# Optimization experiments

Measured on AMD Instinct MI355X. Metric: run time of the kernel, lower is better.

The kernel has to match this reference:

```python
import jax, jax.numpy as jnp
import numpy as np

B, C, N, M, H, L = 2, 128, 6000, 1500, 4, 3
DH = C // H


def conv1(x, W, b):
    # 1x1 Conv1d == per-position matmul: x [B,Cin,N], W [Cout,Cin], b [Cout]
    return jnp.einsum('oc,bcn->bon', W, x) + b[None, :, None]


def setup_inputs():
    key = jax.random.key(0)
    ks = jax.random.split(key, 16)
    w = lambda k, shape, fan: (jax.random.normal(k, shape, jnp.float32) / np.sqrt(fan)).astype(jnp.float32)
    inp = {
        'xs': jax.random.normal(ks[0], (B, 1, N, 4), jnp.float32),
        'd': jax.random.normal(ks[1], (B, C, N), jnp.float32),
        'feat_piece': jax.random.normal(ks[2], (B, C, M), jnp.float32),
        'logits_in': jax.random.normal(ks[3], (B, N), jnp.float32),
        'Wq': w(ks[4], (L, C, C), C), 'bq': jnp.zeros((L, C), jnp.float32),
        'Wk': w(ks[5], (L, C, C), C), 'bk': jnp.zeros((L, C), jnp.float32),
        'Wv': w(ks[6], (L, C, C), C), 'bv': jnp.zeros((L, C), jnp.float32),
        'Wm': w(ks[7], (L, C, C), C), 'bm': jnp.zeros((L, C), jnp.float32),
        'Wc1': w(ks[8], (L, 2 * C, 2 * C), 2 * C), 'bc1': jnp.zeros((L, 2 * C), jnp.float32),
        'bns': jnp.ones((L, 2 * C), jnp.float32), 'bnsh': jnp.zeros((L, 2 * C), jnp.float32),
        'Wc2': w(ks[9], (L, C, 2 * C), 2 * C), 'bc2': jnp.zeros((L, C), jnp.float32),
        'iW1': w(ks[10], (64, C), C), 'ib1': jnp.zeros((64,), jnp.float32),
        'ibn1s': jnp.ones((64,), jnp.float32), 'ibn1sh': jnp.zeros((64,), jnp.float32),
        'iW2': w(ks[11], (16, 64), 64), 'ib2': jnp.zeros((16,), jnp.float32),
        'ibn2s': jnp.ones((16,), jnp.float32), 'ibn2sh': jnp.zeros((16,), jnp.float32),
        'iW3': w(ks[12], (4, 16), 16), 'ib3': jnp.zeros((4,), jnp.float32),
        'ibn3s': jnp.ones((4,), jnp.float32), 'ibn3sh': jnp.zeros((4,), jnp.float32),
        'iW4': w(ks[13], (1, 4), 4), 'ib4': jnp.zeros((1,), jnp.float32),
    }
    return inp


def _forward(xs, d, feat_piece, logits_in, Wq, bq, Wk, bk, Wv, bv, Wm, bm, Wc1, bc1, bns, bnsh, Wc2, bc2,
             iW1, ib1, ibn1s, ibn1sh, iW2, ib2, ibn2s, ibn2sh, iW3, ib3, ibn3s, ibn3sh, iW4, ib4):
    d_old = d
    # kv_mask = (relu(tanh(logits)) > 0) == (logits > 0)
    mask = logits_in > 0.0

    def attention(x1, x2, kv_mask, i):
        bsz = x1.shape[0]
        q = conv1(x1, Wq[i], bq[i]).reshape(bsz, H, DH, -1)  # [B,H,Dh,Nq]
        k = conv1(x2, Wk[i], bk[i]).reshape(bsz, H, DH, -1)  # [B,H,Dh,Nk]
        v = conv1(x2, Wv[i], bv[i]).reshape(bsz, H, DH, -1)
        QK = jnp.einsum('bhdn,bhdm->bhnm', q, k)
        if kv_mask is not None:
            # masked_fill BEFORE the sqrt(head_dim) scaling, as in the original
            QK = jnp.where(kv_mask[:, None, None, :], QK, jnp.float32(-1e6))
        score = jax.nn.softmax(QK / jnp.float32(np.sqrt(DH)), axis=-1)
        add = jnp.einsum('bhnm,bhdm->bhdn', score, v).reshape(bsz, C, -1)
        add = conv1(add, Wm[i], bm[i])
        h = conv1(jnp.concatenate([x1, add], axis=1), Wc1[i], bc1[i])
        # BatchNorm1d (eval) folded into per-channel scale/shift, then ReLU
        h = jax.nn.relu(h * bns[i][None, :, None] + bnsh[i][None, :, None])
        return x1 + conv1(h, Wc2[i], bc2[i])

    feat = attention(feat_piece, d, mask, 0)   # 'cluster':   feat_piece <- d (masked kv)
    feat = attention(feat, feat, None, 1)      # 'context':   self-attention
    d = attention(d, feat, None, 2)            # 'decluster': d <- feat_piece

    def inst_norm(x, eps=1e-3):
        mu = jnp.mean(x, axis=-1, keepdims=True)
        var = jnp.var(x, axis=-1, keepdims=True)  # biased, matches InstanceNorm1d
        return (x - mu) / jnp.sqrt(var + eps)

    def block(x, W, b, s, sh):
        x = inst_norm(conv1(x, W, b))
        return jax.nn.relu(x * s[None, :, None] + sh[None, :, None])

    x = d - d_old
    x = block(x, iW1, ib1, ibn1s, ibn1sh)
    x = block(x, iW2, ib2, ibn2s, ibn2sh)
    x = block(x, iW3, ib3, ibn3s, ibn3sh)
    logits = conv1(x, iW4, ib4)[:, 0, :]  # squeeze channel dim -> [B,N]
    return d, logits  # e_hat is None (loss=False path)


def reference(xs, d, feat_piece, logits_in, Wq, bq, Wk, bk, Wv, bv, Wm, bm, Wc1, bc1, bns, bnsh, Wc2, bc2,
              iW1, ib1, ibn1s, ibn1sh, iW2, ib2, ibn2s, ibn2sh, iW3, ib3, ibn3s, ibn3sh, iW4, ib4):
    return _forward(xs, d, feat_piece, logits_in, Wq, bq, Wk, bk, Wv, bv, Wm, bm, Wc1, bc1, bns, bnsh, Wc2, bc2,
                    iW1, ib1, ibn1s, ibn1sh, iW2, ib2, ibn2s, ibn2sh, iW3, ib3, ibn3s, ibn3sh, iW4, ib4)
```

## Files before the change

### kernel.cpp

```cpp
#include <hip/hip_runtime.h>
#include <math.h>

#define B_  2
#define C_  128
#define N_  6000
#define M_  1500
#define H_  4
#define DH_ 32

typedef __attribute__((ext_vector_type(8))) short bf16x8;
typedef __attribute__((ext_vector_type(4))) float f32x4;
typedef unsigned short u16;

static __device__ __forceinline__ u16 f2bf(float x) {
    unsigned u = __float_as_uint(x);
    return (u16)((u + 0x7fffu + ((u >> 16) & 1u)) >> 16);
}
#define MFMA(a,b,c) __builtin_amdgcn_mfma_f32_16x16x32_bf16((a),(b),(c),0,0,0)
#define INVS2 (0.17677669529663687f * 1.4426950408889634f)

__global__ __launch_bounds__(256) void prep_kernel(
    const float* __restrict__ Wq, const float* __restrict__ Wk, const float* __restrict__ Wv,
    const float* __restrict__ Wm, const float* __restrict__ Wc1, const float* __restrict__ Wc2,
    const float* __restrict__ iW1,
    u16* __restrict__ wq, u16* __restrict__ wk, u16* __restrict__ wv, u16* __restrict__ wm,
    u16* __restrict__ wc1, u16* __restrict__ wc2, u16* __restrict__ w1,
    float* __restrict__ zstats)
{
    long i = (long)blockIdx.x * 256 + threadIdx.x;
    if (i < 512)    zstats[i] = 0.f;
    if (i < 49152)  { wq[i] = f2bf(Wq[i]); wk[i] = f2bf(Wk[i]);
                      wv[i] = f2bf(Wv[i]); wm[i] = f2bf(Wm[i]); }
    if (i < 196608) wc1[i] = f2bf(Wc1[i]);
    if (i < 98304)  wc2[i] = f2bf(Wc2[i]);
    if (i < 8192)   w1[i]  = f2bf(iW1[i]);
}

__global__ __launch_bounds__(256) void qkv_kernel(
    const float* __restrict__ x1, const float* __restrict__ x2, int Pq, int Pk, int Pkpad,
    const u16* __restrict__ wq, const u16* __restrict__ wk, const u16* __restrict__ wv,
    const float* __restrict__ bq, const float* __restrict__ bk, const float* __restrict__ bv,
    u16* __restrict__ Q16, u16* __restrict__ K16, u16* __restrict__ V16)
{
    __shared__ u16 Xt[64][40];
    const int tid = threadIdx.x;
    const int wid = tid >> 6, lane = tid & 63;
    const int l15 = lane & 15, quad = lane >> 4;
    const int job = blockIdx.y >> 1, ot = blockIdx.y & 1;
    const int b = blockIdx.z;
    const int p0 = blockIdx.x * 64;
    const float* X; const u16* W; const float* bias; u16* Y; int P;
    if (job == 0)      { X = x1; W = wq; bias = bq; Y = Q16; P = Pq; }
    else if (job == 1) { X = x2; W = wk; bias = bk; Y = K16; P = Pk; }
    else               { X = x2; W = wv; bias = bv; Y = V16; P = Pk; }
    if (p0 >= P) return;
    const long xoff = (long)b * C_ * P;
    const int sp = tid & 63, cg = tid >> 6;
    f32x4 acc[4] = {};

    for (int k0 = 0; k0 < 128; k0 += 32) {
        bf16x8 st;
        {
            const int pp = (p0 + sp < P) ? p0 + sp : P - 1;
            #pragma unroll
            for (int j = 0; j < 8; ++j)
                st[j] = (short)f2bf(X[xoff + (long)(k0 + cg * 8 + j) * P + pp]);
        }
        __syncthreads();
        *(bf16x8*)&Xt[sp][cg * 8] = st;
        __syncthreads();
        const bf16x8 af = *(const bf16x8*)(W + (long)(ot * 64 + wid * 16 + l15) * 128 + k0 + quad * 8);
        #pragma unroll
        for (int pg = 0; pg < 4; ++pg) {
            const bf16x8 bfr = *(const bf16x8*)&Xt[pg * 16 + l15][quad * 8];
            acc[pg] = MFMA(af, bfr, acc[pg]);
        }
    }
    #pragma unroll
    for (int pg = 0; pg < 4; ++pg)
        #pragma unroll
        for (int r = 0; r < 4; ++r) {
            const int o = ot * 64 + wid * 16 + quad * 4 + r;
            const int p = p0 + pg * 16 + l15;
            if (p < P) {
                const u16 v = f2bf(acc[pg][r] + bias[o]);
                if (job <= 1)
                    Y[((long)(b * 4 + (o >> 5)) * P + p) * 32 + (o & 31)] = v;
                else
                    Y[(long)(b * 128 + o) * Pkpad + p] = v;
            }
        }
}

__global__ __launch_bounds__(256) void attn_partial(
    const u16* __restrict__ Q16, const u16* __restrict__ K16, const u16* __restrict__ V16,
    const float* __restrict__ lgin,
    float* __restrict__ pl, float* __restrict__ pacc,
    int Nq, int Nk, int Nkpad, int KS, int chunkLen)
{
    __shared__ u16 Ps[4][32][72];
    const int tid  = threadIdx.x;
    const int wave = tid >> 6, lane = tid & 63;
    const int l15  = lane & 15, quad = lane >> 4;
    const int bid  = blockIdx.x;
    const int bh   = bid & 7, rest = bid >> 3;
    const int split = rest % KS, qblk = rest / KS;
    const int b = bh >> 2;
    const int q0w = qblk * 128 + wave * 32;

    const u16* Qb = Q16 + (long)bh * Nq * 32;
    const u16* Kb = K16 + (long)bh * Nk * 32;
    const u16* Vb = V16 + (long)(bh * 32) * Nkpad;

    const int qq0 = min(q0w + l15, Nq - 1);
    const int qq1 = min(q0w + 16 + l15, Nq - 1);
    const bf16x8 qa0 = *(const bf16x8*)(Qb + (long)qq0 * 32 + quad * 8);
    const bf16x8 qa1 = *(const bf16x8*)(Qb + (long)qq1 * 32 + quad * 8);

    float lp0 = 0.f, lp1 = 0.f;
    f32x4 o00 = {0.f,0.f,0.f,0.f}, o01 = {0.f,0.f,0.f,0.f};
    f32x4 o10 = {0.f,0.f,0.f,0.f}, o11 = {0.f,0.f,0.f,0.f};

    const int kbeg = split * chunkLen;
    const int kend = min(Nk, kbeg + chunkLen);
    const f32x4 z4 = {0.f,0.f,0.f,0.f};

    for (int m0 = kbeg; m0 < kend; m0 += 64) {
        f32x4 sa0[4], sa1[4];
        #pragma unroll
        for (int kg = 0; kg < 4; ++kg) {
            const int krow = min(m0 + kg * 16 + l15, Nk - 1);
            const bf16x8 ka = *(const bf16x8*)(Kb + (long)krow * 32 + quad * 8);
            sa0[kg] = MFMA(ka, qa0, z4);
            sa1[kg] = MFMA(ka, qa1, z4);
        }

        const int kedge = kend - m0;
        #pragma unroll
        for (int kg = 0; kg < 4; ++kg) {
            float4 mv = {1.f, 1.f, 1.f, 1.f};
            if (lgin)
                mv = *(const float4*)&lgin[(long)b * Nk + min(m0 + kg * 16 + quad * 4, Nk - 4)];
            const float* mr = (const float*)&mv;
            unsigned lo0, hi0, lo1, hi1;
            float p0[4], p1[4];
            #pragma unroll
            for (int r = 0; r < 4; ++r) {
                const bool good = (kg * 16 + quad * 4 + r < kedge) && (mr[r] > 0.f);
                p0[r] = good ? exp2f(sa0[kg][r] * INVS2) : 0.f;
                p1[r] = good ? exp2f(sa1[kg][r] * INVS2) : 0.f;
            }
            lp0 += (p0[0] + p0[1]) + (p0[2] + p0[3]);
            lp1 += (p1[0] + p1[1]) + (p1[2] + p1[3]);
            lo0 = (unsigned)f2bf(p0[0]) | ((unsigned)f2bf(p0[1]) << 16);
            hi0 = (unsigned)f2bf(p0[2]) | ((unsigned)f2bf(p0[3]) << 16);
            lo1 = (unsigned)f2bf(p1[0]) | ((unsigned)f2bf(p1[1]) << 16);
            hi1 = (unsigned)f2bf(p1[2]) | ((unsigned)f2bf(p1[3]) << 16);
            *(uint2*)&Ps[wave][l15][kg * 16 + quad * 4]      = make_uint2(lo0, hi0);
            *(uint2*)&Ps[wave][16 + l15][kg * 16 + quad * 4] = make_uint2(lo1, hi1);
        }

        const bf16x8 pa0lo = *(const bf16x8*)&Ps[wave][l15][quad * 8];
        const bf16x8 pa0hi = *(const bf16x8*)&Ps[wave][l15][32 + quad * 8];
        const bf16x8 pa1lo = *(const bf16x8*)&Ps[wave][16 + l15][quad * 8];
        const bf16x8 pa1hi = *(const bf16x8*)&Ps[wave][16 + l15][32 + quad * 8];
        #pragma unroll
        for (int dg = 0; dg < 2; ++dg) {
            const u16* vrow = Vb + (long)(dg * 16 + l15) * Nkpad + m0;
            const bf16x8 vblo = *(const bf16x8*)(vrow + quad * 8);
            const bf16x8 vbhi = *(const bf16x8*)(vrow + 32 + quad * 8);
            if (dg == 0) {
                o00 = MFMA(pa0lo, vblo, o00); o00 = MFMA(pa0hi, vbhi, o00);
                o10 = MFMA(pa1lo, vblo, o10); o10 = MFMA(pa1hi, vbhi, o10);
            } else {
                o01 = MFMA(pa0lo, vblo, o01); o01 = MFMA(pa0hi, vbhi, o01);
                o11 = MFMA(pa1lo, vblo, o11); o11 = MFMA(pa1hi, vbhi, o11);
            }
        }
    }

    lp0 += __shfl_xor(lp0, 16); lp0 += __shfl_xor(lp0, 32);
    lp1 += __shfl_xor(lp1, 16); lp1 += __shfl_xor(lp1, 32);

    const long base = (long)bh * KS + split;
    if (quad == 0) {
        const int qa = q0w + l15, qbq = q0w + 16 + l15;
        if (qa  < Nq) pl[base * Nq + qa]  = lp0;
        if (qbq < Nq) pl[base * Nq + qbq] = lp1;
    }
    #pragma unroll
    for (int r = 0; r < 4; ++r) {
        const int qa = q0w + quad * 4 + r;
        const int qbq = q0w + 16 + quad * 4 + r;
        if (qa < Nq) {
            float* dst = &pacc[((long)base * Nq + qa) * 32];
            dst[l15] = o00[r]; dst[16 + l15] = o01[r];
        }
        if (qbq < Nq) {
            float* dst = &pacc[((long)base * Nq + qbq) * 32];
            dst[l15] = o10[r]; dst[16 + l15] = o11[r];
        }
    }
}

__global__ __launch_bounds__(256) void epi_kernel(
    const float* __restrict__ pl, const float* __restrict__ pacc, int KS,
    const float* __restrict__ x1,
    const u16* __restrict__ Wm, const float* __restrict__ bm,
    const u16* __restrict__ Wc1, const float* __restrict__ bc1,
    const float* __restrict__ bns, const float* __restrict__ bnsh,
    const u16* __restrict__ Wc2, const float* __restrict__ bc2,
    float* __restrict__ outF, float* __restrict__ outR, int Nq)
{
    __shared__ u16 Xa[32][136];
    __shared__ u16 Xc[32][264];
    __shared__ u16 Xh[32][264];
    const int tid = threadIdx.x;
    const int wid = tid >> 6, lane = tid & 63;
    const int l15 = lane & 15, quad = lane >> 4;
    const int b = blockIdx.y;
    const int p0 = blockIdx.x * 32;

    {
        const int pos = tid & 31, sub = tid >> 5;
        const int pp = (p0 + pos < Nq) ? p0 + pos : Nq - 1;
        const int h = sub >> 1, d0 = (sub & 1) * 16;
        const int bh = b * 4 + h;
        float lg = 0.f, acc[16];
        #pragma unroll
        for (int i = 0; i < 16; ++i) acc[i] = 0.f;
        for (int s = 0; s < KS; ++s) {
            const long base = (long)bh * KS + s;
            lg += pl[base * Nq + pp];
            const float* src = &pacc[(base * Nq + pp) * 32 + d0];
            #pragma unroll
            for (int i = 0; i < 4; ++i) {
                const float4 v = *(const float4*)&src[i * 4];
                acc[i*4+0] += v.x; acc[i*4+1] += v.y; acc[i*4+2] += v.z; acc[i*4+3] += v.w;
            }
        }
        const float inv = 1.f / lg;
        bf16x8 v0, v1;
        #pragma unroll
        for (int i = 0; i < 8; ++i) { v0[i] = (short)f2bf(acc[i] * inv); v1[i] = (short)f2bf(acc[8 + i] * inv); }
        const int c0 = h * 32 + (sub & 1) * 16;
        *(bf16x8*)&Xa[pos][c0] = v0;
        *(bf16x8*)&Xa[pos][c0 + 8] = v1;
        bf16x8 y0, y1;
        #pragma unroll
        for (int j = 0; j < 8; ++j) {
            y0[j] = (short)f2bf(x1[((long)b * 128 + sub * 16 + j) * Nq + pp]);
            y1[j] = (short)f2bf(x1[((long)b * 128 + sub * 16 + 8 + j) * Nq + pp]);
        }
        *(bf16x8*)&Xc[pos][sub * 16] = y0;
        *(bf16x8*)&Xc[pos][sub * 16 + 8] = y1;
    }
    __syncthreads();

    {
        f32x4 am[2][2] = {};
        for (int k0 = 0; k0 < 128; k0 += 32) {
            #pragma unroll
            for (int og = 0; og < 2; ++og) {
                const bf16x8 af = *(const bf16x8*)(Wm + (long)(wid * 32 + og * 16 + l15) * 128 + k0 + quad * 8);
                #pragma unroll
                for (int pg = 0; pg < 2; ++pg) {
                    const bf16x8 bfr = *(const bf16x8*)&Xa[pg * 16 + l15][k0 + quad * 8];
                    am[og][pg] = MFMA(af, bfr, am[og][pg]);
                }
            }
        }
        #pragma unroll
        for (int og = 0; og < 2; ++og)
            #pragma unroll
            for (int pg = 0; pg < 2; ++pg)
                #pragma unroll
                for (int r = 0; r < 4; ++r) {
                    const int o = wid * 32 + og * 16 + quad * 4 + r;
                    Xc[pg * 16 + l15][128 + o] = f2bf(am[og][pg][r] + bm[o]);
                }
    }
    __syncthreads();

    {
        f32x4 a1[4][2] = {};
        for (int k0 = 0; k0 < 256; k0 += 32) {
            #pragma unroll
            for (int og = 0; og < 4; ++og) {
                const bf16x8 af = *(const bf16x8*)(Wc1 + (long)(wid * 64 + og * 16 + l15) * 256 + k0 + quad * 8);
                #pragma unroll
                for (int pg = 0; pg < 2; ++pg) {
                    const bf16x8 bfr = *(const bf16x8*)&Xc[pg * 16 + l15][k0 + quad * 8];
                    a1[og][pg] = MFMA(af, bfr, a1[og][pg]);
                }
            }
        }
        #pragma unroll
        for (int og = 0; og < 4; ++og)
            #pragma unroll
            for (int pg = 0; pg < 2; ++pg)
                #pragma unroll
                for (int r = 0; r < 4; ++r) {
                    const int o = wid * 64 + og * 16 + quad * 4 + r;
                    const float hv = fmaxf((a1[og][pg][r] + bc1[o]) * bns[o] + bnsh[o], 0.f);
                    Xh[pg * 16 + l15][o] = f2bf(hv);
                }
    }
    __syncthreads();

    {
        f32x4 a2[2][2] = {};
        for (int k0 = 0; k0 < 256; k0 += 32) {
            #pragma unroll
            for (int og = 0; og < 2; ++og) {
                const bf16x8 af = *(const bf16x8*)(Wc2 + (long)(wid * 32 + og * 16 + l15) * 256 + k0 + quad * 8);
                #pragma unroll
                for (int pg = 0; pg < 2; ++pg) {
                    const bf16x8 bfr = *(const bf16x8*)&Xh[pg * 16 + l15][k0 + quad * 8];
                    a2[og][pg] = MFMA(af, bfr, a2[og][pg]);
                }
            }
        }
        #pragma unroll
        for (int og = 0; og < 2; ++og)
            #pragma unroll
            for (int pg = 0; pg < 2; ++pg)
                #pragma unroll
                for (int r = 0; r < 4; ++r) {
                    const int o = wid * 32 + og * 16 + quad * 4 + r;
                    const int p = p0 + pg * 16 + l15;
                    if (p < Nq) {
                        const long idx = ((long)b * 128 + o) * Nq + p;
                        const float v = a2[og][pg][r] + bc2[o];
                        outF[idx] = v + x1[idx];
                        if (outR) outR[idx] = v;
                    }
                }
    }
}

__global__ __launch_bounds__(256) void tail1_kernel(
    const float* __restrict__ X, const u16* __restrict__ W, const float* __restrict__ bias,
    float* __restrict__ Y, float* __restrict__ ps, float* __restrict__ pq, int P)
{
    __shared__ u16 Xt[64][40];
    const int tid = threadIdx.x;
    const int wid = tid >> 6, lane = tid & 63;
    const int l15 = lane & 15, quad = lane >> 4;
    const int b = blockIdx.y;
    const int p0 = blockIdx.x * 64;
    const int sp = tid & 63, cg = tid >> 6;
    f32x4 acc[4] = {};
    for (int k0 = 0; k0 < 128; k0 += 32) {
        bf16x8 st;
        {
            const int pp = (p0 + sp < P) ? p0 + sp : P - 1;
            #pragma unroll
            for (int j = 0; j < 8; ++j)
                st[j] = (short)f2bf(X[((long)b * 128 + k0 + cg * 8 + j) * P + pp]);
        }
        __syncthreads();
        *(bf16x8*)&Xt[sp][cg * 8] = st;
        __syncthreads();
        const bf16x8 af = *(const bf16x8*)(W + (long)(wid * 16 + l15) * 128 + k0 + quad * 8);
        #pragma unroll
        for (int pg = 0; pg < 4; ++pg) {
            const bf16x8 bfr = *(const bf16x8*)&Xt[pg * 16 + l15][quad * 8];
            acc[pg] = MFMA(af, bfr, acc[pg]);
        }
    }
    float sums[4] = {}, sq[4] = {};
    #pragma unroll
    for (int pg = 0; pg < 4; ++pg)
        #pragma unroll
        for (int r = 0; r < 4; ++r) {
            const int o = wid * 16 + quad * 4 + r;
            const int p = p0 + pg * 16 + l15;
            if (p < P) {
                const float v = acc[pg][r] + bias[o];
                Y[((long)b * 64 + o) * P + p] = v;
                sums[r] += v; sq[r] += v * v;
            }
        }
    #pragma unroll
    for (int mk = 1; mk < 16; mk <<= 1)
        #pragma unroll
        for (int r = 0; r < 4; ++r) { sums[r] += __shfl_xor(sums[r], mk); sq[r] += __shfl_xor(sq[r], mk); }
    if (l15 == 0)
        #pragma unroll
        for (int r = 0; r < 4; ++r) {
            const int o = wid * 16 + quad * 4 + r;
            atomicAdd(&ps[b * 64 + o], sums[r]);
            atomicAdd(&pq[b * 64 + o], sq[r]);
        }
}

template<int CI, int CO>
__global__ __launch_bounds__(256) void tail_mid(
    const float* __restrict__ xraw, const float* __restrict__ ps, const float* __restrict__ pq,
    const float* __restrict__ sc, const float* __restrict__ sh,
    const float* __restrict__ W, const float* __restrict__ bias,
    float* __restrict__ ps2, float* __restrict__ pq2, float* __restrict__ yraw, int P)
{
    __shared__ float k1s[CI], k2s[CI], Wl[CO * CI];
    const int tid = threadIdx.x;
    const int b = blockIdx.y;
    for (int i = tid; i < CO * CI; i += 256) Wl[i] = W[i];
    if (tid < CI) {
        const float S = ps[b * CI + tid], Q2 = pq[b * CI + tid];
        const float mu = S / P;
        const float var = Q2 / P - mu * mu;
        const float rs = rsqrtf(var + 1e-3f);
        k1s[tid] = rs * sc[tid];
        k2s[tid] = sh[tid] - mu * rs * sc[tid];
    }
    __syncthreads();
    const int p = blockIdx.x * 256 + tid;
    const bool valid = p < P;
    const int pp = valid ? p : P - 1;
    float acc[CO];
    #pragma unroll
    for (int o = 0; o < CO; ++o) acc[o] = bias[o];
    for (int c = 0; c < CI; ++c) {
        const float xn = fmaxf(xraw[((long)b * CI + c) * P + pp] * k1s[c] + k2s[c], 0.f);
        #pragma unroll
        for (int o = 0; o < CO; ++o) acc[o] += Wl[o * CI + c] * xn;
    }
    float sums[CO], sq[CO];
    #pragma unroll
    for (int o = 0; o < CO; ++o) {
        const float v = acc[o];
        if (valid) yraw[((long)b * CO + o) * P + p] = v;
        sums[o] = valid ? v : 0.f;
        sq[o] = valid ? v * v : 0.f;
    }
    #pragma unroll
    for (int mk = 1; mk < 64; mk <<= 1)
        #pragma unroll
        for (int o = 0; o < CO; ++o) { sums[o] += __shfl_xor(sums[o], mk); sq[o] += __shfl_xor(sq[o], mk); }
    if ((tid & 63) == 0)
        #pragma unroll
        for (int o = 0; o < CO; ++o) {
            atomicAdd(&ps2[b * CO + o], sums[o]);
            atomicAdd(&pq2[b * CO + o], sq[o]);
        }
}

__global__ __launch_bounds__(256) void tail4_kernel(
    const float* __restrict__ xraw, const float* __restrict__ ps, const float* __restrict__ pq,
    const float* __restrict__ sc, const float* __restrict__ sh,
    const float* __restrict__ W4, const float* __restrict__ b4,
    float* __restrict__ out, int P)
{
    const int tid = threadIdx.x;
    const int b = blockIdx.y;
    const int p = blockIdx.x * 256 + tid;
    if (p >= P) return;
    float acc = b4[0];
    #pragma unroll
    for (int c = 0; c < 4; ++c) {
        const float S = ps[b * 4 + c], Q2 = pq[b * 4 + c];
        const float mu = S / P;
        const float var = Q2 / P - mu * mu;
        const float rs = rsqrtf(var + 1e-3f);
        const float k1 = rs * sc[c], k2 = sh[c] - mu * rs * sc[c];
        const float xn = fmaxf(xraw[((long)b * 4 + c) * P + p] * k1 + k2, 0.f);
        acc += W4[c] * xn;
    }
    out[(long)b * P + p] = acc;
}

extern "C" void kernel_launch(void* const* d_in, const int* in_sizes, int n_in,
                              void* d_out, int out_size, void* d_ws, size_t ws_size,
                              hipStream_t stream)
{
    const float* dX   = (const float*)d_in[1];
    const float* fpX  = (const float*)d_in[2];
    const float* lgin = (const float*)d_in[3];
    const float* Wq = (const float*)d_in[4];  const float* bq = (const float*)d_in[5];
    const float* Wk = (const float*)d_in[6];  const float* bk = (const float*)d_in[7];
    const float* Wv = (const float*)d_in[8];  const float* bv = (const float*)d_in[9];
    const float* Wm = (const float*)d_in[10]; const float* bm = (const float*)d_in[11];
    const float* Wc1= (const float*)d_in[12]; const float* bc1= (const float*)d_in[13];
    const float* bns= (const float*)d_in[14]; const float* bnsh=(const float*)d_in[15];
    const float* Wc2= (const float*)d_in[16]; const float* bc2= (const float*)d_in[17];
    const float* iW1= (const float*)d_in[18]; const float* ib1= (const float*)d_in[19];
    const float* s1 = (const float*)d_in[20]; const float* h1 = (const float*)d_in[21];
    const float* iW2= (const float*)d_in[22]; const float* ib2= (const float*)d_in[23];
    const float* s2 = (const float*)d_in[24]; const float* h2 = (const float*)d_in[25];
    const float* iW3= (const float*)d_in[26]; const float* ib3= (const float*)d_in[27];
    const float* s3 = (const float*)d_in[28]; const float* h3 = (const float*)d_in[29];
    const float* iW4= (const float*)d_in[30]; const float* ib4= (const float*)d_in[31];

    float* out_d      = (float*)d_out;
    float* out_logits = out_d + (long)B_ * C_ * N_;

    float* f = (float*)d_ws;
    long off = 0;
    auto alloc = [&](long n) { float* p = f + off; off += n; return p; };
    float* featA = alloc(384000);
    float* featB = alloc(384000);
    float* q16f  = alloc(800000);
    float* k16f  = alloc(800000);
    float* v16f  = alloc(800000);
    float* xb    = alloc(1536000);
    float* x1raw = alloc(768000);
    float* x2raw = alloc(192000);
    float* x3raw = alloc(48000);
    float* plb   = alloc(100000);
    float* pacc  = alloc(3200000);
    float* zst   = alloc(512);
    float* wreg  = alloc(250000);
    (void)ws_size; (void)in_sizes; (void)n_in; (void)out_size;

    float* ps1 = zst;        float* pq1 = zst + 128;
    float* ps2 = zst + 256;  float* pq2 = zst + 288;
    float* ps3 = zst + 320;  float* pq3 = zst + 328;

    u16* wq_h  = (u16*)wreg;
    u16* wk_h  = wq_h + 49152;
    u16* wv_h  = wk_h + 49152;
    u16* wm_h  = wv_h + 49152;
    u16* wc1_h = wm_h + 49152;
    u16* wc2_h = wc1_h + 196608;
    u16* w1_h  = wc2_h + 98304;

    u16* Q16 = (u16*)q16f;
    u16* K16 = (u16*)k16f;
    u16* V16 = (u16*)v16f;

    prep_kernel<<<dim3(768), 256, 0, stream>>>(Wq, Wk, Wv, Wm, Wc1, Wc2, iW1,
                                               wq_h, wk_h, wv_h, wm_h, wc1_h, wc2_h, w1_h, zst);

    auto layer = [&](const float* x1, const float* x2, int Nq, int Nk,
                     const float* maskl, int li, int KS, int chunkLen,
                     float* outF, float* outR) {
        const int Nkpad = ((Nk + 63) & ~63) + 64;
        qkv_kernel<<<dim3((max(Nq, Nk) + 63) / 64, 6, B_), 256, 0, stream>>>(
            x1, x2, Nq, Nk, Nkpad,
            wq_h + (long)li * 16384, wk_h + (long)li * 16384, wv_h + (long)li * 16384,
            bq + li * 128, bk + li * 128, bv + li * 128, Q16, K16, V16);
        const int qblocks = (Nq + 127) / 128;
        attn_partial<<<dim3(qblocks * KS * 8), 256, 0, stream>>>(
            Q16, K16, V16, maskl, plb, pacc, Nq, Nk, Nkpad, KS, chunkLen);
        epi_kernel<<<dim3((Nq + 31) / 32, B_), 256, 0, stream>>>(
            plb, pacc, KS, x1,
            wm_h + (long)li * 16384, bm + li * 128,
            wc1_h + (long)li * 65536, bc1 + li * 256, bns + li * 256, bnsh + li * 256,
            wc2_h + (long)li * 32768, bc2 + li * 128,
            outF, outR, Nq);
    };

    layer(fpX,   dX,    M_, N_, lgin,    0, 8, 768, featA, nullptr);
    layer(featA, featA, M_, M_, nullptr, 1, 8, 192, featB, nullptr);
    layer(dX,    featB, N_, M_, nullptr, 2, 2, 768, out_d, xb);

    tail1_kernel<<<dim3((N_ + 63) / 64, B_), 256, 0, stream>>>(xb, w1_h, ib1, x1raw, ps1, pq1, N_);
    tail_mid<64, 16><<<dim3((N_ + 255) / 256, B_), 256, 0, stream>>>(
        x1raw, ps1, pq1, s1, h1, iW2, ib2, ps2, pq2, x2raw, N_);
    tail_mid<16, 4><<<dim3((N_ + 255) / 256, B_), 256, 0, stream>>>(
        x2raw, ps2, pq2, s2, h2, iW3, ib3, ps3, pq3, x3raw, N_);
    tail4_kernel<<<dim3((N_ + 255) / 256, B_), 256, 0, stream>>>(
        x3raw, ps3, pq3, s3, h3, iW4, ib4, out_logits, N_);
}
```

Measured before the change: 397.8 us.

## Pad K/V to chunk size, fold softmax scale into Q, fuse tail kernels

The QKV projection now pre-scales Q by the softmax constant and zero-pads K and V to the full split length. V also gets a row of ones, so the attention kernel can drop per-key bounds checks and compute the softmax row sums with MFMA instead of shuffles. The attention kernel is templated on masking, so the unmasked layers skip the logit loads. The four tail kernels are merged into one persistent 96-block kernel that uses atomic-counter grid barriers between the instance-norm stages. This cuts launch overhead, but the barriers need every block resident at once and add spin-wait cost.

```diff
diff --git a/kernel.cpp b/kernel.cpp
--- a/kernel.cpp
+++ b/kernel.cpp
@@ -49,54 +49,71 @@
     const int job = blockIdx.y >> 1, ot = blockIdx.y & 1;
     const int b = blockIdx.z;
     const int p0 = blockIdx.x * 64;
-    const float* X; const u16* W; const float* bias; u16* Y; int P;
-    if (job == 0)      { X = x1; W = wq; bias = bq; Y = Q16; P = Pq; }
-    else if (job == 1) { X = x2; W = wk; bias = bk; Y = K16; P = Pk; }
-    else               { X = x2; W = wv; bias = bv; Y = V16; P = Pk; }
-    if (p0 >= P) return;
-    const long xoff = (long)b * C_ * P;
-    const int sp = tid & 63, cg = tid >> 6;
-    f32x4 acc[4] = {};
-
-    for (int k0 = 0; k0 < 128; k0 += 32) {
-        bf16x8 st;
-        {
-            const int pp = (p0 + sp < P) ? p0 + sp : P - 1;
-            #pragma unroll
-            for (int j = 0; j < 8; ++j)
-                st[j] = (short)f2bf(X[xoff + (long)(k0 + cg * 8 + j) * P + pp]);
-        }
-        __syncthreads();
-        *(bf16x8*)&Xt[sp][cg * 8] = st;
-        __syncthreads();
-        const bf16x8 af = *(const bf16x8*)(W + (long)(ot * 64 + wid * 16 + l15) * 128 + k0 + quad * 8);
-        #pragma unroll
-        for (int pg = 0; pg < 4; ++pg) {
-            const bf16x8 bfr = *(const bf16x8*)&Xt[pg * 16 + l15][quad * 8];
-            acc[pg] = MFMA(af, bfr, acc[pg]);
-        }
-    }
-    #pragma unroll
-    for (int pg = 0; pg < 4; ++pg)
-        #pragma unroll
-        for (int r = 0; r < 4; ++r) {
-            const int o = ot * 64 + wid * 16 + quad * 4 + r;
-            const int p = p0 + pg * 16 + l15;
-            if (p < P) {
-                const u16 v = f2bf(acc[pg][r] + bias[o]);
-                if (job <= 1)
-                    Y[((long)(b * 4 + (o >> 5)) * P + p) * 32 + (o & 31)] = v;
-                else
-                    Y[(long)(b * 128 + o) * Pkpad + p] = v;
-            }
-        }
-}
-
+    const float* X; const u16* W; const float* bias; int P;
+    if (job == 0)      { X = x1; W = wq; bias = bq; P = Pq; }
+    else if (job == 1) { X = x2; W = wk; bias = bk; P = Pk; }
+    else               { X = x2; W = wv; bias = bv; P = Pk; }
+    const int Plim = (job == 0) ? Pq : Pkpad;
+    if (p0 < Plim) {
+        const long xoff = (long)b * C_ * P;
+        const int sp = tid & 63, cg = tid >> 6;
+        f32x4 acc[4] = {};
+        if (p0 < P) {
+            for (int k0 = 0; k0 < 128; k0 += 32) {
+                bf16x8 st;
+                const int pp = (p0 + sp < P) ? p0 + sp : P - 1;
+                #pragma unroll
+                for (int j = 0; j < 8; ++j)
+                    st[j] = (short)f2bf(X[xoff + (long)(k0 + cg * 8 + j) * P + pp]);
+                __syncthreads();
+                *(bf16x8*)&Xt[sp][cg * 8] = st;
+                __syncthreads();
+                const bf16x8 af = *(const bf16x8*)(W + (long)(ot * 64 + wid * 16 + l15) * 128 + k0 + quad * 8);
+                #pragma unroll
+                for (int pg = 0; pg < 4; ++pg) {
+                    const bf16x8 bfr = *(const bf16x8*)&Xt[pg * 16 + l15][quad * 8];
+                    acc[pg] = MFMA(af, bfr, acc[pg]);
+                }
+            }
+        }
+        #pragma unroll
+        for (int pg = 0; pg < 4; ++pg)
+            #pragma unroll
+            for (int r = 0; r < 4; ++r) {
+                const int o = ot * 64 + wid * 16 + quad * 4 + r;
+                const int p = p0 + pg * 16 + l15;
+                if (p >= Plim) continue;
+                if (job == 0) {
+                    if (p < Pq)
+                        Q16[((long)(b * 4 + (o >> 5)) * Pq + p) * 32 + (o & 31)] =
+                            f2bf((acc[pg][r] + bias[o]) * INVS2);
+                } else {
+                    const u16 v = (p < P) ? f2bf(acc[pg][r] + bias[o]) : (u16)0;
+                    if (job == 1)
+                        K16[((long)(b * 4 + (o >> 5)) * Pkpad + p) * 32 + (o & 31)] = v;
+                    else
+                        V16[((long)(b * 4 + (o >> 5)) * 48 + (o & 31)) * Pkpad + p] = v;
+                }
+            }
+        if (job == 2) {
+            for (int e = tid; e < 2048; e += 256) {
+                const int which = e >> 10;
+                const int row = 32 + ((e >> 6) & 15);
+                const int col = p0 + (e & 63);
+                if (col < Pkpad)
+                    V16[((long)(b * 4 + ot * 2 + which) * 48 + row) * Pkpad + col] =
+                        (row == 32) ? (u16)0x3F80 : (u16)0;
+            }
+        }
+    }
+}
+
+template<bool MASKED>
 __global__ __launch_bounds__(256) void attn_partial(
     const u16* __restrict__ Q16, const u16* __restrict__ K16, const u16* __restrict__ V16,
     const float* __restrict__ lgin,
     float* __restrict__ pl, float* __restrict__ pacc,
-    int Nq, int Nk, int Nkpad, int KS, int chunkLen)
+    int Nq, int Nk, int Nkpad, int KS, int chunkLen, int npad)
 {
     __shared__ u16 Ps[4][32][72];
     const int tid  = threadIdx.x;
@@ -109,97 +126,90 @@
     const int q0w = qblk * 128 + wave * 32;
 
     const u16* Qb = Q16 + (long)bh * Nq * 32;
-    const u16* Kb = K16 + (long)bh * Nk * 32;
-    const u16* Vb = V16 + (long)(bh * 32) * Nkpad;
+    const u16* Kb = K16 + (long)bh * Nkpad * 32;
+    const u16* Vb = V16 + (long)(bh * 48) * Nkpad;
 
     const int qq0 = min(q0w + l15, Nq - 1);
     const int qq1 = min(q0w + 16 + l15, Nq - 1);
     const bf16x8 qa0 = *(const bf16x8*)(Qb + (long)qq0 * 32 + quad * 8);
     const bf16x8 qa1 = *(const bf16x8*)(Qb + (long)qq1 * 32 + quad * 8);
 
-    float lp0 = 0.f, lp1 = 0.f;
-    f32x4 o00 = {0.f,0.f,0.f,0.f}, o01 = {0.f,0.f,0.f,0.f};
-    f32x4 o10 = {0.f,0.f,0.f,0.f}, o11 = {0.f,0.f,0.f,0.f};
+    bf16x8 onesf;
+    #pragma unroll
+    for (int j = 0; j < 8; ++j) onesf[j] = (short)(l15 == 0 ? 0x3F80 : 0);
+
+    f32x4 o00={0,0,0,0}, o01={0,0,0,0}, o10={0,0,0,0}, o11={0,0,0,0};
+    f32x4 ol0={0,0,0,0}, ol1={0,0,0,0};
+    const f32x4 z4 = {0,0,0,0};
 
     const int kbeg = split * chunkLen;
-    const int kend = min(Nk, kbeg + chunkLen);
-    const f32x4 z4 = {0.f,0.f,0.f,0.f};
+    const int kend = kbeg + chunkLen;
 
     for (int m0 = kbeg; m0 < kend; m0 += 64) {
         f32x4 sa0[4], sa1[4];
         #pragma unroll
         for (int kg = 0; kg < 4; ++kg) {
-            const int krow = min(m0 + kg * 16 + l15, Nk - 1);
-            const bf16x8 ka = *(const bf16x8*)(Kb + (long)krow * 32 + quad * 8);
+            const bf16x8 ka = *(const bf16x8*)(Kb + (long)(m0 + kg * 16 + l15) * 32 + quad * 8);
             sa0[kg] = MFMA(ka, qa0, z4);
             sa1[kg] = MFMA(ka, qa1, z4);
         }
-
-        const int kedge = kend - m0;
         #pragma unroll
         for (int kg = 0; kg < 4; ++kg) {
-            float4 mv = {1.f, 1.f, 1.f, 1.f};
-            if (lgin)
-                mv = *(const float4*)&lgin[(long)b * Nk + min(m0 + kg * 16 + quad * 4, Nk - 4)];
-            const float* mr = (const float*)&mv;
-            unsigned lo0, hi0, lo1, hi1;
             float p0[4], p1[4];
-            #pragma unroll
-            for (int r = 0; r < 4; ++r) {
-                const bool good = (kg * 16 + quad * 4 + r < kedge) && (mr[r] > 0.f);
-                p0[r] = good ? exp2f(sa0[kg][r] * INVS2) : 0.f;
-                p1[r] = good ? exp2f(sa1[kg][r] * INVS2) : 0.f;
-            }
-            lp0 += (p0[0] + p0[1]) + (p0[2] + p0[3]);
-            lp1 += (p1[0] + p1[1]) + (p1[2] + p1[3]);
-            lo0 = (unsigned)f2bf(p0[0]) | ((unsigned)f2bf(p0[1]) << 16);
-            hi0 = (unsigned)f2bf(p0[2]) | ((unsigned)f2bf(p0[3]) << 16);
-            lo1 = (unsigned)f2bf(p1[0]) | ((unsigned)f2bf(p1[1]) << 16);
-            hi1 = (unsigned)f2bf(p1[2]) | ((unsigned)f2bf(p1[3]) << 16);
-            *(uint2*)&Ps[wave][l15][kg * 16 + quad * 4]      = make_uint2(lo0, hi0);
-            *(uint2*)&Ps[wave][16 + l15][kg * 16 + quad * 4] = make_uint2(lo1, hi1);
-        }
-
+            if (MASKED) {
+                const int kbase = m0 + kg * 16 + quad * 4;
+                const float4 mv = *(const float4*)&lgin[(long)b * Nk + min(kbase, Nk - 4)];
+                const float* mr = (const float*)&mv;
+                #pragma unroll
+                for (int r = 0; r < 4; ++r) {
+                    const bool good = (kbase + r < Nk) && (mr[r] > 0.f);
+                    p0[r] = good ? exp2f(sa0[kg][r]) : 0.f;
+                    p1[r] = good ? exp2f(sa1[kg][r]) : 0.f;
+                }
+            } else {
+                #pragma unroll
+                for (int r = 0; r < 4; ++r) { p0[r] = exp2f(sa0[kg][r]); p1[r] = exp2f(sa1[kg][r]); }
+            }
+            const unsigned a0 = (__float_as_uint(p0[0]) >> 16) | (__float_as_uint(p0[1]) & 0xffff0000u);
+            const unsigned a1 = (__float_as_uint(p0[2]) >> 16) | (__float_as_uint(p0[3]) & 0xffff0000u);
+            const unsigned b0 = (__float_as_uint(p1[0]) >> 16) | (__float_as_uint(p1[1]) & 0xffff0000u);
+            const unsigned b1 = (__float_as_uint(p1[2]) >> 16) | (__float_as_uint(p1[3]) & 0xffff0000u);
+            *(uint2*)&Ps[wave][l15][kg * 16 + quad * 4]      = make_uint2(a0, a1);
+            *(uint2*)&Ps[wave][16 + l15][kg * 16 + quad * 4] = make_uint2(b0, b1);
+        }
         const bf16x8 pa0lo = *(const bf16x8*)&Ps[wave][l15][quad * 8];
         const bf16x8 pa0hi = *(const bf16x8*)&Ps[wave][l15][32 + quad * 8];
         const bf16x8 pa1lo = *(const bf16x8*)&Ps[wave][16 + l15][quad * 8];
         const bf16x8 pa1hi = *(const bf16x8*)&Ps[wave][16 + l15][32 + quad * 8];
-        #pragma unroll
-        for (int dg = 0; dg < 2; ++dg) {
-            const u16* vrow = Vb + (long)(dg * 16 + l15) * Nkpad + m0;
-            const bf16x8 vblo = *(const bf16x8*)(vrow + quad * 8);
-            const bf16x8 vbhi = *(const bf16x8*)(vrow + 32 + quad * 8);
-            if (dg == 0) {
-                o00 = MFMA(pa0lo, vblo, o00); o00 = MFMA(pa0hi, vbhi, o00);
-                o10 = MFMA(pa1lo, vblo, o10); o10 = MFMA(pa1hi, vbhi, o10);
-            } else {
-                o01 = MFMA(pa0lo, vblo, o01); o01 = MFMA(pa0hi, vbhi, o01);
-                o11 = MFMA(pa1lo, vblo, o11); o11 = MFMA(pa1hi, vbhi, o11);
-            }
-        }
-    }
-
-    lp0 += __shfl_xor(lp0, 16); lp0 += __shfl_xor(lp0, 32);
-    lp1 += __shfl_xor(lp1, 16); lp1 += __shfl_xor(lp1, 32);
+        const u16* vr0 = Vb + (long)l15 * Nkpad + m0;
+        const u16* vr1 = Vb + (long)(16 + l15) * Nkpad + m0;
+        const bf16x8 v0lo = *(const bf16x8*)(vr0 + quad * 8);
+        const bf16x8 v0hi = *(const bf16x8*)(vr0 + 32 + quad * 8);
+        const bf16x8 v1lo = *(const bf16x8*)(vr1 + quad * 8);
+        const bf16x8 v1hi = *(const bf16x8*)(vr1 + 32 + quad * 8);
+        o00 = MFMA(pa0lo, v0lo, o00); o00 = MFMA(pa0hi, v0hi, o00);
+        o01 = MFMA(pa0lo, v1lo, o01); o01 = MFMA(pa0hi, v1hi, o01);
+        o10 = MFMA(pa1lo, v0lo, o10); o10 = MFMA(pa1hi, v0hi, o10);
+        o11 = MFMA(pa1lo, v1lo, o11); o11 = MFMA(pa1hi, v1hi, o11);
+        ol0 = MFMA(pa0lo, onesf, ol0); ol0 = MFMA(pa0hi, onesf, ol0);
+        ol1 = MFMA(pa1lo, onesf, ol1); ol1 = MFMA(pa1hi, onesf, ol1);
+    }
 
     const long base = (long)bh * KS + split;
-    if (quad == 0) {
-        const int qa = q0w + l15, qbq = q0w + 16 + l15;
-        if (qa  < Nq) pl[base * Nq + qa]  = lp0;
-        if (qbq < Nq) pl[base * Nq + qbq] = lp1;
+    const float fn = (split == KS - 1) ? (float)npad : 0.f;
+    if (l15 == 0) {
+        #pragma unroll
+        for (int r = 0; r < 4; ++r) {
+            const int qA = q0w + quad * 4 + r, qB = qA + 16;
+            if (qA < Nq) pl[base * Nq + qA] = ol0[r] - fn;
+            if (qB < Nq) pl[base * Nq + qB] = ol1[r] - fn;
+        }
     }
     #pragma unroll
     for (int r = 0; r < 4; ++r) {
-        const int qa = q0w + quad * 4 + r;
-        const int qbq = q0w + 16 + quad * 4 + r;
-        if (qa < Nq) {
-            float* dst = &pacc[((long)base * Nq + qa) * 32];
-            dst[l15] = o00[r]; dst[16 + l15] = o01[r];
-        }
-        if (qbq < Nq) {
-            float* dst = &pacc[((long)base * Nq + qbq) * 32];
-            dst[l15] = o10[r]; dst[16 + l15] = o11[r];
-        }
+        const int qA = q0w + quad * 4 + r, qB = qA + 16;
+        if (qA < Nq) { float* d = &pacc[((long)base * Nq + qA) * 32]; d[l15] = o00[r]; d[16 + l15] = o01[r]; }
+        if (qB < Nq) { float* d = &pacc[((long)base * Nq + qB) * 32]; d[l15] = o10[r]; d[16 + l15] = o11[r]; }
     }
 }
 
@@ -339,135 +349,200 @@
     }
 }
 
-__global__ __launch_bounds__(256) void tail1_kernel(
-    const float* __restrict__ X, const u16* __restrict__ W, const float* __restrict__ bias,
-    float* __restrict__ Y, float* __restrict__ ps, float* __restrict__ pq, int P)
+__device__ __forceinline__ void gbar(unsigned* c, unsigned tgt) {
+    __syncthreads();
+    __threadfence();
+    if (threadIdx.x == 0) {
+        __hip_atomic_fetch_add(c, 1u, __ATOMIC_ACQ_REL, __HIP_MEMORY_SCOPE_AGENT);
+        while (__hip_atomic_load(c, __ATOMIC_ACQUIRE, __HIP_MEMORY_SCOPE_AGENT) < tgt)
+            __builtin_amdgcn_s_sleep(4);
+    }
+    __syncthreads();
+    __threadfence();
+}
+
+__global__ __launch_bounds__(256) void tail_fused(
+    const float* __restrict__ xb, const u16* __restrict__ w1, const float* __restrict__ ib1,
+    const float* __restrict__ s1, const float* __restrict__ h1,
+    const float* __restrict__ iW2, const float* __restrict__ ib2,
+    const float* __restrict__ s2, const float* __restrict__ h2,
+    const float* __restrict__ iW3, const float* __restrict__ ib3,
+    const float* __restrict__ s3, const float* __restrict__ h3,
+    const float* __restrict__ iW4, const float* __restrict__ ib4,
+    float* __restrict__ x1raw, float* __restrict__ x2raw, float* __restrict__ x3raw,
+    float* __restrict__ ps1, float* __restrict__ pq1,
+    float* __restrict__ ps2, float* __restrict__ pq2,
+    float* __restrict__ ps3, float* __restrict__ pq3,
+    unsigned* __restrict__ bars, float* __restrict__ out, int P)
 {
     __shared__ u16 Xt[64][40];
+    __shared__ float k1s[128], k2s[128], Wl[1024];
     const int tid = threadIdx.x;
     const int wid = tid >> 6, lane = tid & 63;
     const int l15 = lane & 15, quad = lane >> 4;
-    const int b = blockIdx.y;
-    const int p0 = blockIdx.x * 64;
-    const int sp = tid & 63, cg = tid >> 6;
-    f32x4 acc[4] = {};
-    for (int k0 = 0; k0 < 128; k0 += 32) {
-        bf16x8 st;
-        {
+    const int G = gridDim.x;
+
+    const int TJ = (P + 63) >> 6;
+    for (int job = blockIdx.x; job < TJ * 2; job += G) {
+        const int b = job / TJ, p0 = (job % TJ) * 64;
+        const int sp = tid & 63, cg = tid >> 6;
+        f32x4 acc[4] = {};
+        for (int k0 = 0; k0 < 128; k0 += 32) {
+            bf16x8 st;
             const int pp = (p0 + sp < P) ? p0 + sp : P - 1;
             #pragma unroll
             for (int j = 0; j < 8; ++j)
-                st[j] = (short)f2bf(X[((long)b * 128 + k0 + cg * 8 + j) * P + pp]);
-        }
+                st[j] = (short)f2bf(xb[((long)b * 128 + k0 + cg * 8 + j) * P + pp]);
+            __syncthreads();
+            *(bf16x8*)&Xt[sp][cg * 8] = st;
+            __syncthreads();
+            const bf16x8 af = *(const bf16x8*)(w1 + (long)(wid * 16 + l15) * 128 + k0 + quad * 8);
+            #pragma unroll
+            for (int pg = 0; pg < 4; ++pg)
+                acc[pg] = MFMA(af, *(const bf16x8*)&Xt[pg * 16 + l15][quad * 8], acc[pg]);
+        }
+        float sums[4] = {}, sq[4] = {};
+        #pragma unroll
+        for (int pg = 0; pg < 4; ++pg)
+            #pragma unroll
+            for (int r = 0; r < 4; ++r) {
+                const int o = wid * 16 + quad * 4 + r;
+                const int p = p0 + pg * 16 + l15;
+                if (p < P) {
+                    const float v = acc[pg][r] + ib1[o];
+                    x1raw[((long)b * 64 + o) * P + p] = v;
+                    sums[r] += v; sq[r] += v * v;
+                }
+            }
+        #pragma unroll
+        for (int mk = 1; mk < 16; mk <<= 1)
+            #pragma unroll
+            for (int r = 0; r < 4; ++r) { sums[r] += __shfl_xor(sums[r], mk); sq[r] += __shfl_xor(sq[r], mk); }
+        if (l15 == 0)
+            #pragma unroll
+            for (int r = 0; r < 4; ++r) {
+                const int o = wid * 16 + quad * 4 + r;
+                atomicAdd(&ps1[b * 64 + o], sums[r]);
+                atomicAdd(&pq1[b * 64 + o], sq[r]);
+            }
         __syncthreads();
-        *(bf16x8*)&Xt[sp][cg * 8] = st;
+    }
+    gbar(&bars[0], G);
+
+    const int half = G >> 1;
+    const int bB = blockIdx.x >= half;
+    const int slot = blockIdx.x - (bB ? half : 0);
+    const int pB = slot * 256 + tid;
+
+    {
+        if (tid < 128) {
+            const int b = tid >> 6, c = tid & 63;
+            const float S  = __hip_atomic_load(&ps1[b * 64 + c], __ATOMIC_ACQUIRE, __HIP_MEMORY_SCOPE_AGENT);
+            const float Q2 = __hip_atomic_load(&pq1[b * 64 + c], __ATOMIC_ACQUIRE, __HIP_MEMORY_SCOPE_AGENT);
+            const float mu = S / P, var = Q2 / P - mu * mu;
+            const float rs = rsqrtf(var + 1e-3f);
+            k1s[tid] = rs * s1[c];
+            k2s[tid] = h1[c] - mu * rs * s1[c];
+        }
+        for (int i = tid; i < 1024; i += 256) Wl[i] = iW2[i];
         __syncthreads();
-        const bf16x8 af = *(const bf16x8*)(W + (long)(wid * 16 + l15) * 128 + k0 + quad * 8);
-        #pragma unroll
-        for (int pg = 0; pg < 4; ++pg) {
-            const bf16x8 bfr = *(const bf16x8*)&Xt[pg * 16 + l15][quad * 8];
-            acc[pg] = MFMA(af, bfr, acc[pg]);
-        }
-    }
-    float sums[4] = {}, sq[4] = {};
-    #pragma unroll
-    for (int pg = 0; pg < 4; ++pg)
-        #pragma unroll
-        for (int r = 0; r < 4; ++r) {
-            const int o = wid * 16 + quad * 4 + r;
-            const int p = p0 + pg * 16 + l15;
-            if (p < P) {
-                const float v = acc[pg][r] + bias[o];
-                Y[((long)b * 64 + o) * P + p] = v;
-                sums[r] += v; sq[r] += v * v;
-            }
-        }
-    #pragma unroll
-    for (int mk = 1; mk < 16; mk <<= 1)
-        #pragma unroll
-        for (int r = 0; r < 4; ++r) { sums[r] += __shfl_xor(sums[r], mk); sq[r] += __shfl_xor(sq[r], mk); }
-    if (l15 == 0)
-        #pragma unroll
-        for (int r = 0; r < 4; ++r) {
-            const int o = wid * 16 + quad * 4 + r;
-            atomicAdd(&ps[b * 64 + o], sums[r]);
-            atomicAdd(&pq[b * 64 + o], sq[r]);
-        }
-}
-
-template<int CI, int CO>
-__global__ __launch_bounds__(256) void tail_mid(
-    const float* __restrict__ xraw, const float* __restrict__ ps, const float* __restrict__ pq,
-    const float* __restrict__ sc, const float* __restrict__ sh,
-    const float* __restrict__ W, const float* __restrict__ bias,
-    float* __restrict__ ps2, float* __restrict__ pq2, float* __restrict__ yraw, int P)
-{
-    __shared__ float k1s[CI], k2s[CI], Wl[CO * CI];
-    const int tid = threadIdx.x;
-    const int b = blockIdx.y;
-    for (int i = tid; i < CO * CI; i += 256) Wl[i] = W[i];
-    if (tid < CI) {
-        const float S = ps[b * CI + tid], Q2 = pq[b * CI + tid];
-        const float mu = S / P;
-        const float var = Q2 / P - mu * mu;
-        const float rs = rsqrtf(var + 1e-3f);
-        k1s[tid] = rs * sc[tid];
-        k2s[tid] = sh[tid] - mu * rs * sc[tid];
-    }
-    __syncthreads();
-    const int p = blockIdx.x * 256 + tid;
-    const bool valid = p < P;
-    const int pp = valid ? p : P - 1;
-    float acc[CO];
-    #pragma unroll
-    for (int o = 0; o < CO; ++o) acc[o] = bias[o];
-    for (int c = 0; c < CI; ++c) {
-        const float xn = fmaxf(xraw[((long)b * CI + c) * P + pp] * k1s[c] + k2s[c], 0.f);
-        #pragma unroll
-        for (int o = 0; o < CO; ++o) acc[o] += Wl[o * CI + c] * xn;
-    }
-    float sums[CO], sq[CO];
-    #pragma unroll
-    for (int o = 0; o < CO; ++o) {
-        const float v = acc[o];
-        if (valid) yraw[((long)b * CO + o) * P + p] = v;
-        sums[o] = valid ? v : 0.f;
-        sq[o] = valid ? v * v : 0.f;
-    }
-    #pragma unroll
-    for (int mk = 1; mk < 64; mk <<= 1)
-        #pragma unroll
-        for (int o = 0; o < CO; ++o) { sums[o] += __shfl_xor(sums[o], mk); sq[o] += __shfl_xor(sq[o], mk); }
-    if ((tid & 63) == 0)
-        #pragma unroll
-        for (int o = 0; o < CO; ++o) {
-            atomicAdd(&ps2[b * CO + o], sums[o]);
-            atomicAdd(&pq2[b * CO + o], sq[o]);
-        }
-}
-
-__global__ __launch_bounds__(256) void tail4_kernel(
-    const float* __restrict__ xraw, const float* __restrict__ ps, const float* __restrict__ pq,
-    const float* __restrict__ sc, const float* __restrict__ sh,
-    const float* __restrict__ W4, const float* __restrict__ b4,
-    float* __restrict__ out, int P)
-{
-    const int tid = threadIdx.x;
-    const int b = blockIdx.y;
-    const int p = blockIdx.x * 256 + tid;
-    if (p >= P) return;
-    float acc = b4[0];
-    #pragma unroll
-    for (int c = 0; c < 4; ++c) {
-        const float S = ps[b * 4 + c], Q2 = pq[b * 4 + c];
-        const float mu = S / P;
-        const float var = Q2 / P - mu * mu;
-        const float rs = rsqrtf(var + 1e-3f);
-        const float k1 = rs * sc[c], k2 = sh[c] - mu * rs * sc[c];
-        const float xn = fmaxf(xraw[((long)b * 4 + c) * P + p] * k1 + k2, 0.f);
-        acc += W4[c] * xn;
-    }
-    out[(long)b * P + p] = acc;
+        float acc[16];
+        #pragma unroll
+        for (int o = 0; o < 16; ++o) acc[o] = ib2[o];
+        if (pB < P) {
+            for (int c = 0; c < 64; ++c) {
+                const float xn = fmaxf(x1raw[((long)bB * 64 + c) * P + pB] * k1s[bB * 64 + c] + k2s[bB * 64 + c], 0.f);
+                #pragma unroll
+                for (int o = 0; o < 16; ++o) acc[o] += Wl[o * 64 + c] * xn;
+            }
+        }
+        float sums[16], sq[16];
+        #pragma unroll
+        for (int o = 0; o < 16; ++o) {
+            const float v = acc[o];
+            if (pB < P) x2raw[((long)bB * 16 + o) * P + pB] = v;
+            sums[o] = (pB < P) ? v : 0.f;
+            sq[o]   = (pB < P) ? v * v : 0.f;
+        }
+        #pragma unroll
+        for (int mk = 1; mk < 64; mk <<= 1)
+            #pragma unroll
+            for (int o = 0; o < 16; ++o) { sums[o] += __shfl_xor(sums[o], mk); sq[o] += __shfl_xor(sq[o], mk); }
+        if (lane == 0)
+            #pragma unroll
+            for (int o = 0; o < 16; ++o) {
+                atomicAdd(&ps2[bB * 16 + o], sums[o]);
+                atomicAdd(&pq2[bB * 16 + o], sq[o]);
+            }
+    }
+    gbar(&bars[1], G);
+
+    {
+        __syncthreads();
+        if (tid < 32) {
+            const int b = tid >> 4, c = tid & 15;
+            const float S  = __hip_atomic_load(&ps2[b * 16 + c], __ATOMIC_ACQUIRE, __HIP_MEMORY_SCOPE_AGENT);
+            const float Q2 = __hip_atomic_load(&pq2[b * 16 + c], __ATOMIC_ACQUIRE, __HIP_MEMORY_SCOPE_AGENT);
+            const float mu = S / P, var = Q2 / P - mu * mu;
+            const float rs = rsqrtf(var + 1e-3f);
+            k1s[tid] = rs * s2[c];
+            k2s[tid] = h2[c] - mu * rs * s2[c];
+        }
+        for (int i = tid; i < 64; i += 256) Wl[i] = iW3[i];
+        __syncthreads();
+        float acc[4];
+        #pragma unroll
+        for (int o = 0; o < 4; ++o) acc[o] = ib3[o];
+        if (pB < P) {
+            for (int c = 0; c < 16; ++c) {
+                const float xn = fmaxf(x2raw[((long)bB * 16 + c) * P + pB] * k1s[bB * 16 + c] + k2s[bB * 16 + c], 0.f);
+                #pragma unroll
+                for (int o = 0; o < 4; ++o) acc[o] += Wl[o * 16 + c] * xn;
+            }
+        }
+        float sums[4], sq[4];
+        #pragma unroll
+        for (int o = 0; o < 4; ++o) {
+            const float v = acc[o];
+            if (pB < P) x3raw[((long)bB * 4 + o) * P + pB] = v;
+            sums[o] = (pB < P) ? v : 0.f;
+            sq[o]   = (pB < P) ? v * v : 0.f;
+        }
+        #pragma unroll
+        for (int mk = 1; mk < 64; mk <<= 1)
+            #pragma unroll
+            for (int o = 0; o < 4; ++o) { sums[o] += __shfl_xor(sums[o], mk); sq[o] += __shfl_xor(sq[o], mk); }
+        if (lane == 0)
+            #pragma unroll
+            for (int o = 0; o < 4; ++o) {
+                atomicAdd(&ps3[bB * 4 + o], sums[o]);
+                atomicAdd(&pq3[bB * 4 + o], sq[o]);
+            }
+    }
+    gbar(&bars[2], G);
+
+    {
+        __syncthreads();
+        if (tid < 8) {
+            const int b = tid >> 2, c = tid & 3;
+            const float S  = __hip_atomic_load(&ps3[b * 4 + c], __ATOMIC_ACQUIRE, __HIP_MEMORY_SCOPE_AGENT);
+            const float Q2 = __hip_atomic_load(&pq3[b * 4 + c], __ATOMIC_ACQUIRE, __HIP_MEMORY_SCOPE_AGENT);
+            const float mu = S / P, var = Q2 / P - mu * mu;
+            const float rs = rsqrtf(var + 1e-3f);
+            k1s[tid] = rs * s3[c];
+            k2s[tid] = h3[c] - mu * rs * s3[c];
+        }
+        __syncthreads();
+        if (pB < P) {
+            float acc = ib4[0];
+            #pragma unroll
+            for (int c = 0; c < 4; ++c) {
+                const float xn = fmaxf(x3raw[((long)bB * 4 + c) * P + pB] * k1s[bB * 4 + c] + k2s[bB * 4 + c], 0.f);
+                acc += iW4[c] * xn;
+            }
+            out[(long)bB * P + pB] = acc;
+        }
+    }
 }
 
 extern "C" void kernel_launch(void* const* d_in, const int* in_sizes, int n_in,
@@ -502,7 +577,7 @@
     float* featB = alloc(384000);
     float* q16f  = alloc(800000);
     float* k16f  = alloc(800000);
-    float* v16f  = alloc(800000);
+    float* v16f  = alloc(1200000);
     float* xb    = alloc(1536000);
     float* x1raw = alloc(768000);
     float* x2raw = alloc(192000);
@@ -516,6 +591,7 @@
     float* ps1 = zst;        float* pq1 = zst + 128;
     float* ps2 = zst + 256;  float* pq2 = zst + 288;
     float* ps3 = zst + 320;  float* pq3 = zst + 328;
+    unsigned* bars = (unsigned*)(zst + 336);
 
     u16* wq_h  = (u16*)wreg;
     u16* wk_h  = wq_h + 49152;
@@ -535,14 +611,19 @@
     auto layer = [&](const float* x1, const float* x2, int Nq, int Nk,
                      const float* maskl, int li, int KS, int chunkLen,
                      float* outF, float* outR) {
-        const int Nkpad = ((Nk + 63) & ~63) + 64;
-        qkv_kernel<<<dim3((max(Nq, Nk) + 63) / 64, 6, B_), 256, 0, stream>>>(
+        const int Nkpad = KS * chunkLen;
+        const int npad  = maskl ? 0 : (Nkpad - Nk);
+        qkv_kernel<<<dim3((max(Nq, Nkpad) + 63) / 64, 6, B_), 256, 0, stream>>>(
             x1, x2, Nq, Nk, Nkpad,
             wq_h + (long)li * 16384, wk_h + (long)li * 16384, wv_h + (long)li * 16384,
             bq + li * 128, bk + li * 128, bv + li * 128, Q16, K16, V16);
         const int qblocks = (Nq + 127) / 128;
-        attn_partial<<<dim3(qblocks * KS * 8), 256, 0, stream>>>(
-            Q16, K16, V16, maskl, plb, pacc, Nq, Nk, Nkpad, KS, chunkLen);
+        if (maskl)
+            attn_partial<true><<<dim3(qblocks * KS * 8), 256, 0, stream>>>(
+                Q16, K16, V16, maskl, plb, pacc, Nq, Nk, Nkpad, KS, chunkLen, npad);
+        else
+            attn_partial<false><<<dim3(qblocks * KS * 8), 256, 0, stream>>>(
+                Q16, K16, V16, nullptr, plb, pacc, Nq, Nk, Nkpad, KS, chunkLen, npad);
         epi_kernel<<<dim3((Nq + 31) / 32, B_), 256, 0, stream>>>(
             plb, pacc, KS, x1,
             wm_h + (long)li * 16384, bm + li * 128,
@@ -555,11 +636,7 @@
     layer(featA, featA, M_, M_, nullptr, 1, 8, 192, featB, nullptr);
     layer(dX,    featB, N_, M_, nullptr, 2, 2, 768, out_d, xb);
 
-    tail1_kernel<<<dim3((N_ + 63) / 64, B_), 256, 0, stream>>>(xb, w1_h, ib1, x1raw, ps1, pq1, N_);
-    tail_mid<64, 16><<<dim3((N_ + 255) / 256, B_), 256, 0, stream>>>(
-        x1raw, ps1, pq1, s1, h1, iW2, ib2, ps2, pq2, x2raw, N_);
-    tail_mid<16, 4><<<dim3((N_ + 255) / 256, B_), 256, 0, stream>>>(
-        x2raw, ps2, pq2, s2, h2, iW3, ib3, ps3, pq3, x3raw, N_);
-    tail4_kernel<<<dim3((N_ + 255) / 256, B_), 256, 0, stream>>>(
-        x3raw, ps3, pq3, s3, h3, iW4, ib4, out_logits, N_);
-}
+    tail_fused<<<dim3(96), 256, 0, stream>>>(
+        xb, w1_h, ib1, s1, h1, iW2, ib2, s2, h2, iW3, ib3, s3, h3, iW4, ib4,
+        x1raw, x2raw, x3raw, ps1, pq1, ps2, pq2, ps3, pq3, bars, out_logits, N_);
+}
```

After: 471.9 us. 18.6% more time.
